# Kernel tuning notes

Hardware: AMD Instinct MI355X
Metric: run time of the kernel (lower is better)

Reference implementation:

```python
import jax, jax.numpy as jnp
import numpy as np

COS_EPS = 1e-6      # torch CosineSimilarity eps
NORM_EPS = 1e-12    # F.normalize default eps
NUM_HEADS = 4
TOPK = 5


def setup_inputs() -> dict:
    key = jax.random.key(0)
    ks = jax.random.split(key, 12)
    B, S, D_in, D = 32, 256, 768, 1024
    N = 50000
    sc = 0.02
    return {
        "hidden": jax.random.normal(ks[0], (B, S, D_in), jnp.float32),
        "table": jax.random.normal(ks[1], (N, D), jnp.float32),
        "fc1_w": jax.random.normal(ks[2], (D, D_in), jnp.float32) * sc,
        "fc1_b": jax.random.normal(ks[3], (D,), jnp.float32) * sc,
        "q_w": jax.random.normal(ks[4], (D, D), jnp.float32) * sc,
        "q_b": jax.random.normal(ks[5], (D,), jnp.float32) * sc,
        "k_w": jax.random.normal(ks[6], (D, D), jnp.float32) * sc,
        "k_b": jax.random.normal(ks[7], (D,), jnp.float32) * sc,
        "v_w": jax.random.normal(ks[8], (D, D), jnp.float32) * sc,
        "v_b": jax.random.normal(ks[9], (D,), jnp.float32) * sc,
        "out_w": jax.random.normal(ks[10], (D, D), jnp.float32) * sc,
        "out_b": jax.random.normal(ks[11], (D,), jnp.float32) * sc,
    }


def reference(hidden, table, fc1_w, fc1_b, q_w, q_b, k_w, k_b, v_w, v_b, out_w, out_b):
    B, S, _ = hidden.shape
    D = fc1_w.shape[0]
    H = NUM_HEADS
    hd = D // H

    # fc1 over last BERT hidden states: [B,S,1024]
    x = jnp.einsum("bsi,di->bsd", hidden, fc1_w) + fc1_b

    # ---- per-sample retrieval (vectorized over batch) ----
    m = jnp.mean(x, axis=1)                       # [B,D] mean over seq
    tn = jnp.linalg.norm(table, axis=1)           # [N]
    mn = jnp.linalg.norm(m, axis=1)               # [B]
    sim = (m @ table.T) / (jnp.maximum(mn, COS_EPS)[:, None]
                           * jnp.maximum(tn, COS_EPS)[None, :])  # [B,N]
    best = jnp.argmax(sim, axis=1)                # [B] top-1 cosine match

    tab_n = table / jnp.maximum(tn, NORM_EPS)[:, None]  # L2-normalized table
    sel = tab_n[best]                             # [B,D]
    # squared euclidean distance, expanded form (avoids [B,N,D] intermediate)
    d2 = (jnp.sum(sel * sel, axis=1)[:, None]
          - 2.0 * (sel @ tab_n.T)
          + jnp.sum(tab_n * tab_n, axis=1)[None, :])  # [B,N]
    _, idx = jax.lax.top_k(-d2, TOPK)             # 5 smallest distances
    targets = table[idx]                          # [B,5,D] (unnormalized rows)

    # ---- torch.nn.MultiheadAttention(query=targets, key=x, value=x) ----
    q = (jnp.einsum("bqd,ed->bqe", targets, q_w) + q_b).reshape(B, TOPK, H, hd)
    k = (jnp.einsum("bsd,ed->bse", x, k_w) + k_b).reshape(B, S, H, hd)
    v = (jnp.einsum("bsd,ed->bse", x, v_w) + v_b).reshape(B, S, H, hd)
    scores = jnp.einsum("bqhd,bkhd->bhqk", q, k) / jnp.sqrt(jnp.asarray(hd, x.dtype))
    attn = jax.nn.softmax(scores, axis=-1)        # [B,H,5,S]
    o = jnp.einsum("bhqk,bkhd->bqhd", attn, v).reshape(B, TOPK, D)
    attn_out = jnp.einsum("bqe,de->bqd", o, out_w) + out_b  # [B,5,D]

    return jnp.sum(attn_out, axis=1)              # [B,D]
```

## Files before the change

kernel.cpp:

```cpp
#include <hip/hip_runtime.h>
#include <stdint.h>

typedef short bf16x8 __attribute__((ext_vector_type(8)));
typedef float f32x4 __attribute__((ext_vector_type(4)));

#define NROWS 50000
#define BATCH 32
#define SEQ 256
#define DIN 768
#define DMODEL 1024
#define NTOPK 5
#define DOTS_RG 782
#define CHUNKF 64
#define NCHUNK_HALF 8

__device__ inline unsigned short f2bf(float f) {
  union { float f; unsigned u; } x; x.f = f;
  unsigned u = x.u;
  unsigned r = u + 0x7fffu + ((u >> 16) & 1u);
  return (unsigned short)(r >> 16);
}
__device__ inline float bf2f(unsigned short h) {
  union { unsigned u; float f; } x; x.u = ((unsigned)h) << 16; return x.f;
}
__device__ inline ushort4 cvt_hi4(float4 f) {
  ushort4 h; h.x = f2bf(f.x); h.y = f2bf(f.y); h.z = f2bf(f.z); h.w = f2bf(f.w); return h;
}
__device__ inline ushort4 cvt_lo4(float4 f, ushort4 h) {
  ushort4 l;
  l.x = f2bf(f.x - bf2f(h.x)); l.y = f2bf(f.y - bf2f(h.y));
  l.z = f2bf(f.z - bf2f(h.z)); l.w = f2bf(f.w - bf2f(h.w));
  return l;
}

__device__ __forceinline__ void gl_lds16(const void* g, void* l) {
  __builtin_amdgcn_global_load_lds(
      (const __attribute__((address_space(1))) unsigned int*)g,
      (__attribute__((address_space(3))) unsigned int*)l, 16, 0, 0);
}

__global__ void k_f32_to_bf16(const float* __restrict__ in, unsigned short* __restrict__ out, int n) {
  int i = (blockIdx.x * blockDim.x + threadIdx.x) * 4;
  int stride = gridDim.x * blockDim.x * 4;
  for (; i < n; i += stride) {
    float4 f = *(const float4*)(in + i);
    ushort4 o;
    o.x = f2bf(f.x); o.y = f2bf(f.y); o.z = f2bf(f.z); o.w = f2bf(f.w);
    *(ushort4*)(out + i) = o;
  }
}

__global__ void k_f32_to_bf16_3(const float* __restrict__ i0, unsigned short* __restrict__ o0, int n0,
                                const float* __restrict__ i1, unsigned short* __restrict__ o1, int n1,
                                const float* __restrict__ i2, unsigned short* __restrict__ o2, int n2) {
  int base = (blockIdx.x * blockDim.x + threadIdx.x) * 4;
  int stride = gridDim.x * blockDim.x * 4;
  for (int i = base; i < n0; i += stride) {
    float4 f = *(const float4*)(i0 + i);
    ushort4 o; o.x = f2bf(f.x); o.y = f2bf(f.y); o.z = f2bf(f.z); o.w = f2bf(f.w);
    *(ushort4*)(o0 + i) = o;
  }
  for (int i = base; i < n1; i += stride) {
    float4 f = *(const float4*)(i1 + i);
    ushort4 o; o.x = f2bf(f.x); o.y = f2bf(f.y); o.z = f2bf(f.z); o.w = f2bf(f.w);
    *(ushort4*)(o1 + i) = o;
  }
  for (int i = base; i < n2; i += stride) {
    float4 f = *(const float4*)(i2 + i);
    ushort4 o; o.x = f2bf(f.x); o.y = f2bf(f.y); o.z = f2bf(f.z); o.w = f2bf(f.w);
    *(ushort4*)(o2 + i) = o;
  }
}

__global__ void k_split_q(const float* __restrict__ v, unsigned short* __restrict__ qhi,
                          unsigned short* __restrict__ qlo) {
  int b = blockIdx.x;
  int e0 = threadIdx.x * 4;
  float4 f = *(const float4*)(v + (size_t)b * DMODEL + e0);
  ushort4 h = cvt_hi4(f);
  ushort4 l = cvt_lo4(f, h);
  *(ushort4*)(qhi + (size_t)b * DMODEL + e0) = h;
  *(ushort4*)(qlo + (size_t)b * DMODEL + e0) = l;
}

__global__ void k_mean_part(const float* __restrict__ hidden, float* __restrict__ hpart) {
  int b = blockIdx.x >> 3, tc = blockIdx.x & 7;
  int i = threadIdx.x;
  const float* p = hidden + ((size_t)b * SEQ + tc * 32) * DIN + i;
  float s = 0.f;
  #pragma unroll 4
  for (int t = 0; t < 32; ++t) s += p[t * DIN];
  hpart[((size_t)tc * 32 + b) * DIN + i] = s;
}
__global__ void k_mean_reduce(const float* __restrict__ hpart, float* __restrict__ hm) {
  int b = blockIdx.x;
  int i = threadIdx.x;
  float s = 0.f;
  #pragma unroll
  for (int tc = 0; tc < 8; ++tc) s += hpart[((size_t)tc * 32 + b) * DIN + i];
  hm[b * DIN + i] = s * (1.0f / SEQ);
}

__global__ void k_sgemm_wt(const float* __restrict__ A, const float* __restrict__ W,
                           const float* __restrict__ bias, float* __restrict__ C,
                           int M, int N, int K, float beta) {
  __shared__ float A_l[32][65];
  __shared__ float W_l[64][65];
  int tid = threadIdx.x;
  int tx = tid & 63, ty = tid >> 6;
  int n0 = blockIdx.x * 64, m0 = blockIdx.y * 32;
  float acc[8] = {0.f,0.f,0.f,0.f,0.f,0.f,0.f,0.f};
  for (int k0 = 0; k0 < K; k0 += 64) {
    #pragma unroll
    for (int i = 0; i < 8; ++i) {
      int idx = tid + 256 * i; int r = idx >> 6, c = idx & 63;
      A_l[r][c] = A[(size_t)(m0 + r) * K + k0 + c];
    }
    #pragma unroll
    for (int i = 0; i < 16; ++i) {
      int idx = tid + 256 * i; int r = idx >> 6, c = idx & 63;
      W_l[r][c] = W[(size_t)(n0 + r) * K + k0 + c];
    }
    __syncthreads();
    for (int kk = 0; kk < 64; ++kk) {
      float wv = W_l[tx][kk];
      #pragma unroll
      for (int r = 0; r < 8; ++r) acc[r] += A_l[ty * 8 + r][kk] * wv;
    }
    __syncthreads();
  }
  float bv = bias[n0 + tx] * beta;
  #pragma unroll
  for (int r = 0; r < 8; ++r) C[(size_t)(m0 + ty * 8 + r) * N + n0 + tx] = acc[r] + bv;
}

__global__ __launch_bounds__(256) void k_bf16_gemm(const unsigned short* __restrict__ A,
    const unsigned short* __restrict__ W, const float* __restrict__ bias,
    unsigned short* __restrict__ C, int M, int N, int K) {
  __shared__ unsigned short As[128][32];
  __shared__ unsigned short Ws[128][32];
  int tid = threadIdx.x;
  int wave = tid >> 6, lane = tid & 63;
  int wr = wave >> 1, wc = wave & 1;
  int bm = blockIdx.y * 128, bn = blockIdx.x * 128;
  int srow = lane >> 2;
  int scol = (lane & 3) * 8;
  f32x4 acc[4][4] = {};
  for (int k0 = 0; k0 < K; k0 += 32) {
    #pragma unroll
    for (int j = 0; j < 2; ++j) {
      int r0 = wave * 32 + j * 16;
      gl_lds16(A + (size_t)(bm + r0 + srow) * K + k0 + scol, &As[r0][0]);
      gl_lds16(W + (size_t)(bn + r0 + srow) * K + k0 + scol, &Ws[r0][0]);
    }
    __syncthreads();
    bf16x8 af[4], bfr[4];
    #pragma unroll
    for (int mi = 0; mi < 4; ++mi)
      af[mi] = *(const bf16x8*)(&As[wr * 64 + mi * 16 + (lane & 15)][(lane >> 4) * 8]);
    #pragma unroll
    for (int ni = 0; ni < 4; ++ni)
      bfr[ni] = *(const bf16x8*)(&Ws[wc * 64 + ni * 16 + (lane & 15)][(lane >> 4) * 8]);
    #pragma unroll
    for (int mi = 0; mi < 4; ++mi)
      #pragma unroll
      for (int ni = 0; ni < 4; ++ni)
        acc[mi][ni] = __builtin_amdgcn_mfma_f32_16x16x32_bf16(af[mi], bfr[ni], acc[mi][ni], 0, 0, 0);
    __syncthreads();
  }
  #pragma unroll
  for (int ni = 0; ni < 4; ++ni) {
    int col = bn + wc * 64 + ni * 16 + (lane & 15);
    float bv = bias[col];
    #pragma unroll
    for (int mi = 0; mi < 4; ++mi) {
      #pragma unroll
      for (int j = 0; j < 4; ++j) {
        int row = bm + wr * 64 + mi * 16 + (lane >> 4) * 4 + j;
        C[(size_t)row * N + col] = f2bf(acc[mi][ni][j] + bv);
      }
    }
  }
}

__global__ __launch_bounds__(256, 4) void k_dots(const float* __restrict__ table,
    const unsigned short* __restrict__ qhi, const unsigned short* __restrict__ qlo,
    float* __restrict__ normp, float* __restrict__ dotsg, int pass1) {
  __shared__ unsigned short As_hi[2][64 * 64];
  __shared__ unsigned short As_lo[2][64 * 64];
  __shared__ float npart[64][4];
  float* dot_lds = (float*)&As_hi[0][0];

  int tid = threadIdx.x;
  int wave = tid >> 6, lane = tid & 63;
  int rg = blockIdx.x >> 1, half = blockIdx.x & 1;
  int rbase = rg * 64;
  int kbase = half * 512;

  int r = tid >> 2;
  int q4 = tid & 3;
  int grow = rbase + r; if (grow >= NROWS) grow = NROWS - 1;
  const float* gsrc = table + (size_t)grow * DMODEL + kbase + q4 * 16;
  int wslot0 = ((q4 * 2) ^ (r & 7)) * 8;
  int wslot1 = ((q4 * 2 + 1) ^ (r & 7)) * 8;
  int wbase = r * 64;

  int abase = (wave * 16 + (lane & 15)) * 64;
  int al7 = lane & 7;
  const unsigned short* qh0 = qhi + (size_t)(lane & 15) * DMODEL + (lane >> 4) * 8 + kbase;
  const unsigned short* qh1 = qh0 + 16 * DMODEL;
  const unsigned short* ql0 = qlo + (size_t)(lane & 15) * DMODEL + (lane >> 4) * 8 + kbase;
  const unsigned short* ql1 = ql0 + 16 * DMODEL;

  float accn = 0.f;
  f32x4 acc0 = {}, acc1 = {};
  float4 f0, f1, f2, f3;

  auto LOAD = [&](int k0) {
    f0 = *(const float4*)(gsrc + k0);
    f1 = *(const float4*)(gsrc + k0 + 4);
    f2 = *(const float4*)(gsrc + k0 + 8);
    f3 = *(const float4*)(gsrc + k0 + 12);
  };
  auto WRITE = [&](int buf) {
    ushort4 h0 = cvt_hi4(f0), h1 = cvt_hi4(f1), h2 = cvt_hi4(f2), h3 = cvt_hi4(f3);
    ushort4 l0 = cvt_lo4(f0, h0), l1 = cvt_lo4(f1, h1), l2 = cvt_lo4(f2, h2), l3 = cvt_lo4(f3, h3);
    accn += f0.x*f0.x + f0.y*f0.y + f0.z*f0.z + f0.w*f0.w
          + f1.x*f1.x + f1.y*f1.y + f1.z*f1.z + f1.w*f1.w
          + f2.x*f2.x + f2.y*f2.y + f2.z*f2.z + f2.w*f2.w
          + f3.x*f3.x + f3.y*f3.y + f3.z*f3.z + f3.w*f3.w;
    *(ushort4*)&As_hi[buf][wbase + wslot0]     = h0;
    *(ushort4*)&As_hi[buf][wbase + wslot0 + 4] = h1;
    *(ushort4*)&As_hi[buf][wbase + wslot1]     = h2;
    *(ushort4*)&As_hi[buf][wbase + wslot1 + 4] = h3;
    *(ushort4*)&As_lo[buf][wbase + wslot0]     = l0;
    *(ushort4*)&As_lo[buf][wbase + wslot0 + 4] = l1;
    *(ushort4*)&As_lo[buf][wbase + wslot1]     = l2;
    *(ushort4*)&As_lo[buf][wbase + wslot1 + 4] = l3;
  };

  LOAD(0);
  for (int ch = 0; ch < NCHUNK_HALF; ++ch) {
    int buf = ch & 1;
    int k0 = ch * CHUNKF;
    bf16x8 bh0[2], bh1[2], bl0[2], bl1[2];
    #pragma unroll
    for (int kk = 0; kk < 2; ++kk) {
      int qoff = k0 + kk * 32;
      bh0[kk] = *(const bf16x8*)(qh0 + qoff);
      bh1[kk] = *(const bf16x8*)(qh1 + qoff);
      bl0[kk] = *(const bf16x8*)(ql0 + qoff);
      bl1[kk] = *(const bf16x8*)(ql1 + qoff);
    }
    WRITE(buf);
    if (ch + 1 < NCHUNK_HALF) LOAD(k0 + CHUNKF);
    #pragma unroll
    for (int kk = 0; kk < 2; ++kk) {
      int s = ((kk * 4 + (lane >> 4)) ^ al7) * 8;
      bf16x8 ah = *(const bf16x8*)&As_hi[buf][abase + s];
      bf16x8 al = *(const bf16x8*)&As_lo[buf][abase + s];
      acc0 = __builtin_amdgcn_mfma_f32_16x16x32_bf16(ah, bh0[kk], acc0, 0, 0, 0);
      acc1 = __builtin_amdgcn_mfma_f32_16x16x32_bf16(ah, bh1[kk], acc1, 0, 0, 0);
      acc0 = __builtin_amdgcn_mfma_f32_16x16x32_bf16(ah, bl0[kk], acc0, 0, 0, 0);
      acc1 = __builtin_amdgcn_mfma_f32_16x16x32_bf16(ah, bl1[kk], acc1, 0, 0, 0);
      acc0 = __builtin_amdgcn_mfma_f32_16x16x32_bf16(al, bh0[kk], acc0, 0, 0, 0);
      acc1 = __builtin_amdgcn_mfma_f32_16x16x32_bf16(al, bh1[kk], acc1, 0, 0, 0);
    }
  }

  npart[r][q4] = accn;
  __syncthreads();
  if (pass1 && tid < 64) {
    int rw = rbase + tid;
    if (rw < NROWS) {
      float n2 = npart[tid][0] + npart[tid][1] + npart[tid][2] + npart[tid][3];
      normp[(size_t)half * NROWS + rw] = n2;
    }
  }
  #pragma unroll
  for (int j = 0; j < 4; ++j) {
    int row = wave * 16 + (lane >> 4) * 4 + j;
    dot_lds[((lane & 15)) * 68 + row] = acc0[j];
    dot_lds[(16 + (lane & 15)) * 68 + row] = acc1[j];
  }
  __syncthreads();
  {
    int b = tid >> 3, r0 = (tid & 7) * 8;
    float* dst = dotsg + ((size_t)blockIdx.x * 32 + b) * 64 + r0;
    float4 v0 = *(const float4*)&dot_lds[b * 68 + r0];
    float4 v1 = *(const float4*)&dot_lds[b * 68 + r0 + 4];
    *(float4*)dst = v0;
    *(float4*)(dst + 4) = v1;
  }
}

__global__ void k_comb5(const float* __restrict__ dotsg, const float* __restrict__ normp,
                        float* __restrict__ norm2f, float* __restrict__ candv,
                        int* __restrict__ candi, int pass1, float eps) {
  __shared__ float sc[32 * 68];
  __shared__ float iv_lds[64];
  int rg = blockIdx.x;
  int tid = threadIdx.x;
  if (tid < 64) {
    int rw = rg * 64 + tid;
    int rc = rw < NROWS ? rw : NROWS - 1;
    float n2;
    if (pass1) {
      n2 = normp[rc] + normp[NROWS + rc];
      if (rw < NROWS) norm2f[rw] = n2;
    } else {
      n2 = norm2f[rc];
    }
    iv_lds[tid] = 1.0f / fmaxf(sqrtf(n2), eps);
  }
  __syncthreads();
  {
    int b = tid >> 3, r0 = (tid & 7) * 8;
    const float* p0 = dotsg + ((size_t)(rg * 2 + 0) * 32 + b) * 64 + r0;
    const float* p1 = dotsg + ((size_t)(rg * 2 + 1) * 32 + b) * 64 + r0;
    #pragma unroll
    for (int i = 0; i < 8; ++i)
      sc[b * 68 + r0 + i] = (p0[i] + p1[i]) * iv_lds[r0 + i];
  }
  __syncthreads();
  if (tid < 32) {
    float tv[5]; int ti[5];
    #pragma unroll
    for (int j = 0; j < 5; ++j) { tv[j] = -3.4e38f; ti[j] = 0x7fffffff; }
    int rbase = rg * 64;
    for (int rr = 0; rr < 64; ++rr) {
      int rw = rbase + rr;
      if (rw >= NROWS) break;
      float v = sc[tid * 68 + rr];
      if (v > tv[4] || (v == tv[4] && rw < ti[4])) {
        tv[4] = v; ti[4] = rw;
        #pragma unroll
        for (int j = 4; j > 0; --j) {
          bool sw = (tv[j] > tv[j-1]) || (tv[j] == tv[j-1] && ti[j] < ti[j-1]);
          if (sw) {
            float fv = tv[j]; tv[j] = tv[j-1]; tv[j-1] = fv;
            int ivx = ti[j]; ti[j] = ti[j-1]; ti[j-1] = ivx;
          }
        }
      }
    }
    #pragma unroll
    for (int j = 0; j < 5; ++j) {
      candv[((size_t)rg * 32 + tid) * 5 + j] = tv[j];
      candi[((size_t)rg * 32 + tid) * 5 + j] = ti[j];
    }
  }
}

__global__ void k_merge(const float* __restrict__ candv, const int* __restrict__ candi,
                        int* __restrict__ out_idx, int K, int nblk) {
  int b = blockIdx.x;
  int tid = threadIdx.x;
  float tv[5]; int ti[5];
  #pragma unroll
  for (int j = 0; j < 5; ++j) { tv[j] = -3.4e38f; ti[j] = 0x7fffffff; }
  for (int blk = tid; blk < nblk; blk += 256) {
    #pragma unroll
    for (int j = 0; j < 5; ++j) {
      float v = candv[((size_t)blk * 32 + b) * 5 + j];
      int idx = candi[((size_t)blk * 32 + b) * 5 + j];
      if (v > tv[4] || (v == tv[4] && idx < ti[4])) {
        tv[4] = v; ti[4] = idx;
        #pragma unroll
        for (int jj = 4; jj > 0; --jj) {
          bool sw = (tv[jj] > tv[jj-1]) || (tv[jj] == tv[jj-1] && ti[jj] < ti[jj-1]);
          if (sw) {
            float fv = tv[jj]; tv[jj] = tv[jj-1]; tv[jj-1] = fv;
            int ivx = ti[jj]; ti[jj] = ti[jj-1]; ti[jj-1] = ivx;
          }
        }
      }
    }
  }
  __shared__ float lv[256 * 5];
  __shared__ int   li[256 * 5];
  #pragma unroll
  for (int j = 0; j < 5; ++j) { lv[tid * 5 + j] = tv[j]; li[tid * 5 + j] = ti[j]; }
  __syncthreads();
  for (int off = 128; off >= 1; off >>= 1) {
    if (tid < off) {
      float av[5], bv[5]; int ai[5], bi[5];
      #pragma unroll
      for (int j = 0; j < 5; ++j) {
        av[j] = lv[tid * 5 + j]; ai[j] = li[tid * 5 + j];
        bv[j] = lv[(tid + off) * 5 + j]; bi[j] = li[(tid + off) * 5 + j];
      }
      int pa = 0, pb = 0;
      float mv[5]; int mi[5];
      #pragma unroll
      for (int j = 0; j < 5; ++j) {
        bool ta = (av[pa] > bv[pb]) || (av[pa] == bv[pb] && ai[pa] < bi[pb]);
        if (ta) { mv[j] = av[pa]; mi[j] = ai[pa]; ++pa; }
        else    { mv[j] = bv[pb]; mi[j] = bi[pb]; ++pb; }
      }
      #pragma unroll
      for (int j = 0; j < 5; ++j) { lv[tid * 5 + j] = mv[j]; li[tid * 5 + j] = mi[j]; }
    }
    __syncthreads();
  }
  if (tid == 0) {
    for (int j = 0; j < K; ++j) out_idx[b * K + j] = li[j];
  }
}

__global__ void k_gather_sel(const float* __restrict__ table, const int* __restrict__ best,
                             float* __restrict__ sel) {
  int b = blockIdx.x, e = threadIdx.x;
  int idx = best[b];
  sel[b * DMODEL + e] = table[(size_t)idx * DMODEL + e];
}

__global__ void k_gather_targets(const float* __restrict__ table, const int* __restrict__ idx5,
                                 float* __restrict__ tg) {
  int bt = blockIdx.x, e = threadIdx.x;
  int idx = idx5[bt];
  tg[(size_t)bt * DMODEL + e] = table[(size_t)idx * DMODEL + e];
}

__global__ __launch_bounds__(256) void k_attention(const float* __restrict__ q,
    const unsigned short* __restrict__ kb, const unsigned short* __restrict__ vb,
    float* __restrict__ obuf) {
  int bt = blockIdx.x;
  int b = bt / NTOPK;
  int tid = threadIdx.x;
  __shared__ float q_l[DMODEL];
  __shared__ float sc[4][SEQ];
  #pragma unroll
  for (int j = 0; j < 4; ++j) q_l[tid + 256 * j] = q[(size_t)bt * DMODEL + tid + 256 * j];
  __syncthreads();
  {
    int s = tid;
    const unsigned short* krow = kb + ((size_t)(b * SEQ + s)) * DMODEL;
    #pragma unroll
    for (int h = 0; h < 4; ++h) {
      float d = 0.f;
      for (int dd = 0; dd < 256; dd += 8) {
        uint4 pk = *(const uint4*)(krow + h * 256 + dd);
        const unsigned short* ph = (const unsigned short*)&pk;
        #pragma unroll
        for (int j2 = 0; j2 < 8; ++j2) d += bf2f(ph[j2]) * q_l[h * 256 + dd + j2];
      }
      sc[h][s] = d * 0.0625f;
    }
  }
  __syncthreads();
  {
    int h = tid >> 6, lane = tid & 63;
    float vals[4];
    float mx = -3.4e38f;
    #pragma unroll
    for (int j = 0; j < 4; ++j) { vals[j] = sc[h][lane + 64 * j]; mx = fmaxf(mx, vals[j]); }
    #pragma unroll
    for (int o = 1; o < 64; o <<= 1) mx = fmaxf(mx, __shfl_xor(mx, o));
    float sum = 0.f;
    #pragma unroll
    for (int j = 0; j < 4; ++j) { vals[j] = expf(vals[j] - mx); sum += vals[j]; }
    #pragma unroll
    for (int o = 1; o < 64; o <<= 1) sum += __shfl_xor(sum, o);
    float rz = 1.0f / sum;
    #pragma unroll
    for (int j = 0; j < 4; ++j) sc[h][lane + 64 * j] = vals[j] * rz;
  }
  __syncthreads();
  {
    int h = tid >> 6;
    int e0 = tid * 4;
    float a0 = 0.f, a1 = 0.f, a2 = 0.f, a3 = 0.f;
    const unsigned short* vbase = vb + (size_t)(b * SEQ) * DMODEL + e0;
    for (int s = 0; s < SEQ; ++s) {
      float w = sc[h][s];
      ushort4 v4 = *(const ushort4*)(vbase + (size_t)s * DMODEL);
      a0 += w * bf2f(v4.x); a1 += w * bf2f(v4.y); a2 += w * bf2f(v4.z); a3 += w * bf2f(v4.w);
    }
    float* op = obuf + (size_t)bt * DMODEL + e0;
    op[0] = a0; op[1] = a1; op[2] = a2; op[3] = a3;
  }
}

__global__ void k_osum(const float* __restrict__ obuf, float* __restrict__ osum) {
  int g = blockIdx.x * blockDim.x + threadIdx.x;
  if (g >= BATCH * DMODEL) return;
  int b = g >> 10, e = g & 1023;
  float s = 0.f;
  #pragma unroll
  for (int t = 0; t < NTOPK; ++t) s += obuf[(size_t)(b * NTOPK + t) * DMODEL + e];
  osum[g] = s;
}

extern "C" void kernel_launch(void* const* d_in, const int* in_sizes, int n_in,
                              void* d_out, int out_size, void* d_ws, size_t ws_size,
                              hipStream_t stream) {
  const float* hidden = (const float*)d_in[0];
  const float* table  = (const float*)d_in[1];
  const float* fc1_w  = (const float*)d_in[2];
  const float* fc1_b  = (const float*)d_in[3];
  const float* q_w    = (const float*)d_in[4];
  const float* q_b    = (const float*)d_in[5];
  const float* k_w    = (const float*)d_in[6];
  const float* k_b    = (const float*)d_in[7];
  const float* v_w    = (const float*)d_in[8];
  const float* v_b    = (const float*)d_in[9];
  const float* out_w  = (const float*)d_in[10];
  const float* out_b  = (const float*)d_in[11];
  float* out = (float*)d_out;

  char* ws = (char*)d_ws;
  size_t off = 0;
  auto alloc = [&](size_t bytes) -> void* {
    void* p = ws + off;
    off += (bytes + 255) & ~(size_t)255;
    return p;
  };
  unsigned short* hid_bf  = (unsigned short*)alloc((size_t)BATCH * SEQ * DIN * 2);
  unsigned short* fc1w_bf = (unsigned short*)alloc((size_t)DMODEL * DIN * 2);
  unsigned short* kw_bf   = (unsigned short*)alloc((size_t)DMODEL * DMODEL * 2);
  unsigned short* vw_bf   = (unsigned short*)alloc((size_t)DMODEL * DMODEL * 2);
  unsigned short* x_bf    = (unsigned short*)alloc((size_t)BATCH * SEQ * DMODEL * 2);
  unsigned short* k_bf    = (unsigned short*)alloc((size_t)BATCH * SEQ * DMODEL * 2);
  unsigned short* v_bf    = (unsigned short*)alloc((size_t)BATCH * SEQ * DMODEL * 2);
  unsigned short* qhi     = (unsigned short*)alloc((size_t)BATCH * DMODEL * 2);
  unsigned short* qlo     = (unsigned short*)alloc((size_t)BATCH * DMODEL * 2);
  float* hpart   = (float*)alloc((size_t)8 * BATCH * DIN * 4);
  float* hm      = (float*)alloc((size_t)BATCH * DIN * 4);
  float* m       = (float*)alloc((size_t)BATCH * DMODEL * 4);
  float* sel     = (float*)alloc((size_t)BATCH * DMODEL * 4);
  float* normp   = (float*)alloc((size_t)2 * NROWS * 4);
  float* norm2f  = (float*)alloc((size_t)NROWS * 4);
  float* dotsg   = (float*)alloc((size_t)DOTS_RG * 2 * 32 * 64 * 4);
  float* candv   = (float*)alloc((size_t)DOTS_RG * 32 * 5 * 4);
  int*   candi   = (int*)alloc((size_t)DOTS_RG * 32 * 5 * 4);
  int*   best    = (int*)alloc(BATCH * 4);
  int*   idx5    = (int*)alloc(BATCH * NTOPK * 4);
  float* targets = (float*)alloc((size_t)BATCH * NTOPK * DMODEL * 4);
  float* qbuf    = (float*)alloc((size_t)BATCH * NTOPK * DMODEL * 4);
  float* obuf    = (float*)alloc((size_t)BATCH * NTOPK * DMODEL * 4);
  float* osum    = (float*)alloc((size_t)BATCH * DMODEL * 4);
  (void)ws_size; (void)in_sizes; (void)n_in; (void)out_size;

  k_f32_to_bf16<<<2048, 256, 0, stream>>>(hidden, hid_bf, BATCH * SEQ * DIN);
  k_f32_to_bf16_3<<<1024, 256, 0, stream>>>(fc1_w, fc1w_bf, DMODEL * DIN,
                                            k_w, kw_bf, DMODEL * DMODEL,
                                            v_w, vw_bf, DMODEL * DMODEL);

  k_mean_part<<<256, 768, 0, stream>>>(hidden, hpart);
  k_mean_reduce<<<32, 768, 0, stream>>>(hpart, hm);
  k_sgemm_wt<<<dim3(16, 1), 256, 0, stream>>>(hm, fc1_w, fc1_b, m, 32, DMODEL, DIN, 1.0f);

  k_bf16_gemm<<<dim3(8, 64), 256, 0, stream>>>(hid_bf, fc1w_bf, fc1_b, x_bf, BATCH * SEQ, DMODEL, DIN);

  k_split_q<<<32, 256, 0, stream>>>(m, qhi, qlo);
  k_dots<<<DOTS_RG * 2, 256, 0, stream>>>(table, qhi, qlo, normp, dotsg, 1);
  k_comb5<<<DOTS_RG, 256, 0, stream>>>(dotsg, normp, norm2f, candv, candi, 1, 1e-6f);
  k_merge<<<32, 256, 0, stream>>>(candv, candi, best, 1, DOTS_RG);
  k_gather_sel<<<32, 1024, 0, stream>>>(table, best, sel);

  k_split_q<<<32, 256, 0, stream>>>(sel, qhi, qlo);
  k_dots<<<DOTS_RG * 2, 256, 0, stream>>>(table, qhi, qlo, normp, dotsg, 0);
  k_comb5<<<DOTS_RG, 256, 0, stream>>>(dotsg, normp, norm2f, candv, candi, 0, 1e-12f);
  k_merge<<<32, 256, 0, stream>>>(candv, candi, idx5, NTOPK, DOTS_RG);
  k_gather_targets<<<160, 1024, 0, stream>>>(table, idx5, targets);

  k_sgemm_wt<<<dim3(16, 5), 256, 0, stream>>>(targets, q_w, q_b, qbuf, BATCH * NTOPK, DMODEL, DMODEL, 1.0f);

  k_bf16_gemm<<<dim3(8, 64), 256, 0, stream>>>(x_bf, kw_bf, k_b, k_bf, BATCH * SEQ, DMODEL, DMODEL);
  k_bf16_gemm<<<dim3(8, 64), 256, 0, stream>>>(x_bf, vw_bf, v_b, v_bf, BATCH * SEQ, DMODEL, DMODEL);

  k_attention<<<160, 256, 0, stream>>>(qbuf, k_bf, v_bf, obuf);
  k_osum<<<128, 256, 0, stream>>>(obuf, osum);
  k_sgemm_wt<<<dim3(16, 1), 256, 0, stream>>>(osum, out_w, out_b, out, 32, DMODEL, DMODEL, 5.0f);
}
```

Measured before the change: 584.2 us.

## Fuse small prep, merge, gather and split kernels; cut k_dots LDS for occupancy

The hidden-state bf16 conversion now shares one pass with the per-chunk seq sum, so hidden is read once instead of twice. The q hi/lo split moves into the fc1 sgemm epilogue and into a combined merge+gather kernel, and the top-5 merge writes targets directly. The osum reduction moves into the out-proj sgemm A-load. k_dots drops LDS double-buffering to a single buffer, raises launch bounds to 6 blocks, and loads the q fragments inside the inner loop. Fewer launches and more resident blocks are traded against less overlap of LDS writes with MFMA reads in k_dots.

```diff
diff --git a/kernel.cpp b/kernel.cpp
--- a/kernel.cpp
+++ b/kernel.cpp
@@ -39,15 +39,29 @@
       (__attribute__((address_space(3))) unsigned int*)l, 16, 0, 0);
 }
 
-__global__ void k_f32_to_bf16(const float* __restrict__ in, unsigned short* __restrict__ out, int n) {
-  int i = (blockIdx.x * blockDim.x + threadIdx.x) * 4;
-  int stride = gridDim.x * blockDim.x * 4;
-  for (; i < n; i += stride) {
-    float4 f = *(const float4*)(in + i);
-    ushort4 o;
-    o.x = f2bf(f.x); o.y = f2bf(f.y); o.z = f2bf(f.z); o.w = f2bf(f.w);
-    *(ushort4*)(out + i) = o;
-  }
+__global__ void k_hidden_prep(const float* __restrict__ hidden, unsigned short* __restrict__ hid_bf,
+                              float* __restrict__ hpart) {
+  int b = blockIdx.x >> 3, tc = blockIdx.x & 7;
+  int i = threadIdx.x;
+  const float* p = hidden + ((size_t)b * SEQ + tc * 32) * DIN + i;
+  unsigned short* o = hid_bf + ((size_t)b * SEQ + tc * 32) * DIN + i;
+  float s = 0.f;
+  #pragma unroll 4
+  for (int t = 0; t < 32; ++t) {
+    float v = p[t * DIN];
+    s += v;
+    o[t * DIN] = f2bf(v);
+  }
+  hpart[((size_t)tc * 32 + b) * DIN + i] = s;
+}
+
+__global__ void k_mean_reduce(const float* __restrict__ hpart, float* __restrict__ hm) {
+  int b = blockIdx.x;
+  int i = threadIdx.x;
+  float s = 0.f;
+  #pragma unroll
+  for (int tc = 0; tc < 8; ++tc) s += hpart[((size_t)tc * 32 + b) * DIN + i];
+  hm[b * DIN + i] = s * (1.0f / SEQ);
 }
 
 __global__ void k_f32_to_bf16_3(const float* __restrict__ i0, unsigned short* __restrict__ o0, int n0,
@@ -72,38 +86,10 @@
   }
 }
 
-__global__ void k_split_q(const float* __restrict__ v, unsigned short* __restrict__ qhi,
-                          unsigned short* __restrict__ qlo) {
-  int b = blockIdx.x;
-  int e0 = threadIdx.x * 4;
-  float4 f = *(const float4*)(v + (size_t)b * DMODEL + e0);
-  ushort4 h = cvt_hi4(f);
-  ushort4 l = cvt_lo4(f, h);
-  *(ushort4*)(qhi + (size_t)b * DMODEL + e0) = h;
-  *(ushort4*)(qlo + (size_t)b * DMODEL + e0) = l;
-}
-
-__global__ void k_mean_part(const float* __restrict__ hidden, float* __restrict__ hpart) {
-  int b = blockIdx.x >> 3, tc = blockIdx.x & 7;
-  int i = threadIdx.x;
-  const float* p = hidden + ((size_t)b * SEQ + tc * 32) * DIN + i;
-  float s = 0.f;
-  #pragma unroll 4
-  for (int t = 0; t < 32; ++t) s += p[t * DIN];
-  hpart[((size_t)tc * 32 + b) * DIN + i] = s;
-}
-__global__ void k_mean_reduce(const float* __restrict__ hpart, float* __restrict__ hm) {
-  int b = blockIdx.x;
-  int i = threadIdx.x;
-  float s = 0.f;
-  #pragma unroll
-  for (int tc = 0; tc < 8; ++tc) s += hpart[((size_t)tc * 32 + b) * DIN + i];
-  hm[b * DIN + i] = s * (1.0f / SEQ);
-}
-
 __global__ void k_sgemm_wt(const float* __restrict__ A, const float* __restrict__ W,
                            const float* __restrict__ bias, float* __restrict__ C,
-                           int M, int N, int K, float beta) {
+                           int M, int N, int K, float beta, int sum5,
+                           unsigned short* __restrict__ qhi, unsigned short* __restrict__ qlo) {
   __shared__ float A_l[32][65];
   __shared__ float W_l[64][65];
   int tid = threadIdx.x;
@@ -114,7 +100,15 @@
     #pragma unroll
     for (int i = 0; i < 8; ++i) {
       int idx = tid + 256 * i; int r = idx >> 6, c = idx & 63;
-      A_l[r][c] = A[(size_t)(m0 + r) * K + k0 + c];
+      if (sum5) {
+        float s = 0.f;
+        #pragma unroll
+        for (int t = 0; t < 5; ++t)
+          s += A[((size_t)(m0 + r) * 5 + t) * K + k0 + c];
+        A_l[r][c] = s;
+      } else {
+        A_l[r][c] = A[(size_t)(m0 + r) * K + k0 + c];
+      }
     }
     #pragma unroll
     for (int i = 0; i < 16; ++i) {
@@ -131,7 +125,16 @@
   }
   float bv = bias[n0 + tx] * beta;
   #pragma unroll
-  for (int r = 0; r < 8; ++r) C[(size_t)(m0 + ty * 8 + r) * N + n0 + tx] = acc[r] + bv;
+  for (int r = 0; r < 8; ++r) {
+    int row = m0 + ty * 8 + r, col = n0 + tx;
+    float v = acc[r] + bv;
+    C[(size_t)row * N + col] = v;
+    if (qhi) {
+      unsigned short h = f2bf(v);
+      qhi[(size_t)row * N + col] = h;
+      qlo[(size_t)row * N + col] = f2bf(v - bf2f(h));
+    }
+  }
 }
 
 __global__ __launch_bounds__(256) void k_bf16_gemm(const unsigned short* __restrict__ A,
@@ -183,13 +186,12 @@
   }
 }
 
-__global__ __launch_bounds__(256, 4) void k_dots(const float* __restrict__ table,
+__global__ __launch_bounds__(256, 6) void k_dots(const float* __restrict__ table,
     const unsigned short* __restrict__ qhi, const unsigned short* __restrict__ qlo,
     float* __restrict__ normp, float* __restrict__ dotsg, int pass1) {
-  __shared__ unsigned short As_hi[2][64 * 64];
-  __shared__ unsigned short As_lo[2][64 * 64];
+  __shared__ unsigned short As[2][64 * 64];
   __shared__ float npart[64][4];
-  float* dot_lds = (float*)&As_hi[0][0];
+  float* dot_lds = (float*)&As[0][0];
 
   int tid = threadIdx.x;
   int wave = tid >> 6, lane = tid & 63;
@@ -222,49 +224,44 @@
     f2 = *(const float4*)(gsrc + k0 + 8);
     f3 = *(const float4*)(gsrc + k0 + 12);
   };
-  auto WRITE = [&](int buf) {
+  auto WRITE = [&]() {
     ushort4 h0 = cvt_hi4(f0), h1 = cvt_hi4(f1), h2 = cvt_hi4(f2), h3 = cvt_hi4(f3);
     ushort4 l0 = cvt_lo4(f0, h0), l1 = cvt_lo4(f1, h1), l2 = cvt_lo4(f2, h2), l3 = cvt_lo4(f3, h3);
     accn += f0.x*f0.x + f0.y*f0.y + f0.z*f0.z + f0.w*f0.w
           + f1.x*f1.x + f1.y*f1.y + f1.z*f1.z + f1.w*f1.w
           + f2.x*f2.x + f2.y*f2.y + f2.z*f2.z + f2.w*f2.w
           + f3.x*f3.x + f3.y*f3.y + f3.z*f3.z + f3.w*f3.w;
-    *(ushort4*)&As_hi[buf][wbase + wslot0]     = h0;
-    *(ushort4*)&As_hi[buf][wbase + wslot0 + 4] = h1;
-    *(ushort4*)&As_hi[buf][wbase + wslot1]     = h2;
-    *(ushort4*)&As_hi[buf][wbase + wslot1 + 4] = h3;
-    *(ushort4*)&As_lo[buf][wbase + wslot0]     = l0;
-    *(ushort4*)&As_lo[buf][wbase + wslot0 + 4] = l1;
-    *(ushort4*)&As_lo[buf][wbase + wslot1]     = l2;
-    *(ushort4*)&As_lo[buf][wbase + wslot1 + 4] = l3;
+    *(ushort4*)&As[0][wbase + wslot0]     = h0;
+    *(ushort4*)&As[0][wbase + wslot0 + 4] = h1;
+    *(ushort4*)&As[0][wbase + wslot1]     = h2;
+    *(ushort4*)&As[0][wbase + wslot1 + 4] = h3;
+    *(ushort4*)&As[1][wbase + wslot0]     = l0;
+    *(ushort4*)&As[1][wbase + wslot0 + 4] = l1;
+    *(ushort4*)&As[1][wbase + wslot1]     = l2;
+    *(ushort4*)&As[1][wbase + wslot1 + 4] = l3;
   };
 
   LOAD(0);
   for (int ch = 0; ch < NCHUNK_HALF; ++ch) {
-    int buf = ch & 1;
     int k0 = ch * CHUNKF;
-    bf16x8 bh0[2], bh1[2], bl0[2], bl1[2];
-    #pragma unroll
-    for (int kk = 0; kk < 2; ++kk) {
-      int qoff = k0 + kk * 32;
-      bh0[kk] = *(const bf16x8*)(qh0 + qoff);
-      bh1[kk] = *(const bf16x8*)(qh1 + qoff);
-      bl0[kk] = *(const bf16x8*)(ql0 + qoff);
-      bl1[kk] = *(const bf16x8*)(ql1 + qoff);
-    }
-    WRITE(buf);
+    WRITE();
     if (ch + 1 < NCHUNK_HALF) LOAD(k0 + CHUNKF);
     #pragma unroll
     for (int kk = 0; kk < 2; ++kk) {
       int s = ((kk * 4 + (lane >> 4)) ^ al7) * 8;
-      bf16x8 ah = *(const bf16x8*)&As_hi[buf][abase + s];
-      bf16x8 al = *(const bf16x8*)&As_lo[buf][abase + s];
-      acc0 = __builtin_amdgcn_mfma_f32_16x16x32_bf16(ah, bh0[kk], acc0, 0, 0, 0);
-      acc1 = __builtin_amdgcn_mfma_f32_16x16x32_bf16(ah, bh1[kk], acc1, 0, 0, 0);
-      acc0 = __builtin_amdgcn_mfma_f32_16x16x32_bf16(ah, bl0[kk], acc0, 0, 0, 0);
-      acc1 = __builtin_amdgcn_mfma_f32_16x16x32_bf16(ah, bl1[kk], acc1, 0, 0, 0);
-      acc0 = __builtin_amdgcn_mfma_f32_16x16x32_bf16(al, bh0[kk], acc0, 0, 0, 0);
-      acc1 = __builtin_amdgcn_mfma_f32_16x16x32_bf16(al, bh1[kk], acc1, 0, 0, 0);
+      bf16x8 ah = *(const bf16x8*)&As[0][abase + s];
+      bf16x8 al = *(const bf16x8*)&As[1][abase + s];
+      int qoff = k0 + kk * 32;
+      bf16x8 bh0 = *(const bf16x8*)(qh0 + qoff);
+      bf16x8 bh1 = *(const bf16x8*)(qh1 + qoff);
+      bf16x8 bl0 = *(const bf16x8*)(ql0 + qoff);
+      bf16x8 bl1 = *(const bf16x8*)(ql1 + qoff);
+      acc0 = __builtin_amdgcn_mfma_f32_16x16x32_bf16(ah, bh0, acc0, 0, 0, 0);
+      acc1 = __builtin_amdgcn_mfma_f32_16x16x32_bf16(ah, bh1, acc1, 0, 0, 0);
+      acc0 = __builtin_amdgcn_mfma_f32_16x16x32_bf16(ah, bl0, acc0, 0, 0, 0);
+      acc1 = __builtin_amdgcn_mfma_f32_16x16x32_bf16(ah, bl1, acc1, 0, 0, 0);
+      acc0 = __builtin_amdgcn_mfma_f32_16x16x32_bf16(al, bh0, acc0, 0, 0, 0);
+      acc1 = __builtin_amdgcn_mfma_f32_16x16x32_bf16(al, bh1, acc1, 0, 0, 0);
     }
   }
 
@@ -352,14 +349,46 @@
   }
 }
 
-__global__ void k_merge(const float* __restrict__ candv, const int* __restrict__ candi,
-                        int* __restrict__ out_idx, int K, int nblk) {
+__global__ void k_mg_split(const float* __restrict__ candv, const int* __restrict__ candi,
+                           const float* __restrict__ table, unsigned short* __restrict__ qhi,
+                           unsigned short* __restrict__ qlo) {
   int b = blockIdx.x;
   int tid = threadIdx.x;
+  float bv = -3.4e38f; int bi = 0x7fffffff;
+  for (int blk = tid; blk < DOTS_RG; blk += 256) {
+    float v = candv[((size_t)blk * 32 + b) * 5];
+    int idx = candi[((size_t)blk * 32 + b) * 5];
+    if (v > bv || (v == bv && idx < bi)) { bv = v; bi = idx; }
+  }
+  __shared__ float sv[256];
+  __shared__ int   si[256];
+  sv[tid] = bv; si[tid] = bi;
+  __syncthreads();
+  for (int off = 128; off >= 1; off >>= 1) {
+    if (tid < off) {
+      float v2 = sv[tid + off]; int i2 = si[tid + off];
+      if (v2 > sv[tid] || (v2 == sv[tid] && i2 < si[tid])) { sv[tid] = v2; si[tid] = i2; }
+    }
+    __syncthreads();
+  }
+  int best = si[0];
+  const float* row = table + (size_t)best * DMODEL;
+  int e0 = tid * 4;
+  float4 f = *(const float4*)(row + e0);
+  ushort4 h = cvt_hi4(f);
+  ushort4 l = cvt_lo4(f, h);
+  *(ushort4*)(qhi + (size_t)b * DMODEL + e0) = h;
+  *(ushort4*)(qlo + (size_t)b * DMODEL + e0) = l;
+}
+
+__global__ void k_mg5(const float* __restrict__ candv, const int* __restrict__ candi,
+                      const float* __restrict__ table, float* __restrict__ targets) {
+  int b = blockIdx.x;
+  int tid = threadIdx.x;
   float tv[5]; int ti[5];
   #pragma unroll
   for (int j = 0; j < 5; ++j) { tv[j] = -3.4e38f; ti[j] = 0x7fffffff; }
-  for (int blk = tid; blk < nblk; blk += 256) {
+  for (int blk = tid; blk < DOTS_RG; blk += 256) {
     #pragma unroll
     for (int j = 0; j < 5; ++j) {
       float v = candv[((size_t)blk * 32 + b) * 5 + j];
@@ -403,23 +432,13 @@
     }
     __syncthreads();
   }
-  if (tid == 0) {
-    for (int j = 0; j < K; ++j) out_idx[b * K + j] = li[j];
-  }
-}
-
-__global__ void k_gather_sel(const float* __restrict__ table, const int* __restrict__ best,
-                             float* __restrict__ sel) {
-  int b = blockIdx.x, e = threadIdx.x;
-  int idx = best[b];
-  sel[b * DMODEL + e] = table[(size_t)idx * DMODEL + e];
-}
-
-__global__ void k_gather_targets(const float* __restrict__ table, const int* __restrict__ idx5,
-                                 float* __restrict__ tg) {
-  int bt = blockIdx.x, e = threadIdx.x;
-  int idx = idx5[bt];
-  tg[(size_t)bt * DMODEL + e] = table[(size_t)idx * DMODEL + e];
+  #pragma unroll
+  for (int j = 0; j < 5; ++j) {
+    int idx = li[j];
+    const float* row = table + (size_t)idx * DMODEL;
+    for (int e = tid * 4; e < DMODEL; e += 1024)
+      *(float4*)(targets + ((size_t)b * NTOPK + j) * DMODEL + e) = *(const float4*)(row + e);
+  }
 }
 
 __global__ __launch_bounds__(256) void k_attention(const float* __restrict__ q,
@@ -480,16 +499,6 @@
     float* op = obuf + (size_t)bt * DMODEL + e0;
     op[0] = a0; op[1] = a1; op[2] = a2; op[3] = a3;
   }
-}
-
-__global__ void k_osum(const float* __restrict__ obuf, float* __restrict__ osum) {
-  int g = blockIdx.x * blockDim.x + threadIdx.x;
-  if (g >= BATCH * DMODEL) return;
-  int b = g >> 10, e = g & 1023;
-  float s = 0.f;
-  #pragma unroll
-  for (int t = 0; t < NTOPK; ++t) s += obuf[(size_t)(b * NTOPK + t) * DMODEL + e];
-  osum[g] = s;
 }
 
 extern "C" void kernel_launch(void* const* d_in, const int* in_sizes, int n_in,
@@ -528,49 +537,42 @@
   float* hpart   = (float*)alloc((size_t)8 * BATCH * DIN * 4);
   float* hm      = (float*)alloc((size_t)BATCH * DIN * 4);
   float* m       = (float*)alloc((size_t)BATCH * DMODEL * 4);
-  float* sel     = (float*)alloc((size_t)BATCH * DMODEL * 4);
   float* normp   = (float*)alloc((size_t)2 * NROWS * 4);
   float* norm2f  = (float*)alloc((size_t)NROWS * 4);
   float* dotsg   = (float*)alloc((size_t)DOTS_RG * 2 * 32 * 64 * 4);
   float* candv   = (float*)alloc((size_t)DOTS_RG * 32 * 5 * 4);
   int*   candi   = (int*)alloc((size_t)DOTS_RG * 32 * 5 * 4);
-  int*   best    = (int*)alloc(BATCH * 4);
-  int*   idx5    = (int*)alloc(BATCH * NTOPK * 4);
   float* targets = (float*)alloc((size_t)BATCH * NTOPK * DMODEL * 4);
   float* qbuf    = (float*)alloc((size_t)BATCH * NTOPK * DMODEL * 4);
   float* obuf    = (float*)alloc((size_t)BATCH * NTOPK * DMODEL * 4);
-  float* osum    = (float*)alloc((size_t)BATCH * DMODEL * 4);
   (void)ws_size; (void)in_sizes; (void)n_in; (void)out_size;
 
-  k_f32_to_bf16<<<2048, 256, 0, stream>>>(hidden, hid_bf, BATCH * SEQ * DIN);
+  k_hidden_prep<<<256, 768, 0, stream>>>(hidden, hid_bf, hpart);
   k_f32_to_bf16_3<<<1024, 256, 0, stream>>>(fc1_w, fc1w_bf, DMODEL * DIN,
                                             k_w, kw_bf, DMODEL * DMODEL,
                                             v_w, vw_bf, DMODEL * DMODEL);
-
-  k_mean_part<<<256, 768, 0, stream>>>(hidden, hpart);
   k_mean_reduce<<<32, 768, 0, stream>>>(hpart, hm);
-  k_sgemm_wt<<<dim3(16, 1), 256, 0, stream>>>(hm, fc1_w, fc1_b, m, 32, DMODEL, DIN, 1.0f);
+
+  k_sgemm_wt<<<dim3(16, 1), 256, 0, stream>>>(hm, fc1_w, fc1_b, m, 32, DMODEL, DIN, 1.0f,
+                                              0, qhi, qlo);
 
   k_bf16_gemm<<<dim3(8, 64), 256, 0, stream>>>(hid_bf, fc1w_bf, fc1_b, x_bf, BATCH * SEQ, DMODEL, DIN);
 
-  k_split_q<<<32, 256, 0, stream>>>(m, qhi, qlo);
   k_dots<<<DOTS_RG * 2, 256, 0, stream>>>(table, qhi, qlo, normp, dotsg, 1);
   k_comb5<<<DOTS_RG, 256, 0, stream>>>(dotsg, normp, norm2f, candv, candi, 1, 1e-6f);
-  k_merge<<<32, 256, 0, stream>>>(candv, candi, best, 1, DOTS_RG);
-  k_gather_sel<<<32, 1024, 0, stream>>>(table, best, sel);
-
-  k_split_q<<<32, 256, 0, stream>>>(sel, qhi, qlo);
+  k_mg_split<<<32, 256, 0, stream>>>(candv, candi, table, qhi, qlo);
+
   k_dots<<<DOTS_RG * 2, 256, 0, stream>>>(table, qhi, qlo, normp, dotsg, 0);
   k_comb5<<<DOTS_RG, 256, 0, stream>>>(dotsg, normp, norm2f, candv, candi, 0, 1e-12f);
-  k_merge<<<32, 256, 0, stream>>>(candv, candi, idx5, NTOPK, DOTS_RG);
-  k_gather_targets<<<160, 1024, 0, stream>>>(table, idx5, targets);
-
-  k_sgemm_wt<<<dim3(16, 5), 256, 0, stream>>>(targets, q_w, q_b, qbuf, BATCH * NTOPK, DMODEL, DMODEL, 1.0f);
+  k_mg5<<<32, 256, 0, stream>>>(candv, candi, table, targets);
+
+  k_sgemm_wt<<<dim3(16, 5), 256, 0, stream>>>(targets, q_w, q_b, qbuf, BATCH * NTOPK, DMODEL, DMODEL,
+                                              1.0f, 0, nullptr, nullptr);
 
   k_bf16_gemm<<<dim3(8, 64), 256, 0, stream>>>(x_bf, kw_bf, k_b, k_bf, BATCH * SEQ, DMODEL, DMODEL);
   k_bf16_gemm<<<dim3(8, 64), 256, 0, stream>>>(x_bf, vw_bf, v_b, v_bf, BATCH * SEQ, DMODEL, DMODEL);
 
   k_attention<<<160, 256, 0, stream>>>(qbuf, k_bf, v_bf, obuf);
-  k_osum<<<128, 256, 0, stream>>>(obuf, osum);
-  k_sgemm_wt<<<dim3(16, 1), 256, 0, stream>>>(osum, out_w, out_b, out, 32, DMODEL, DMODEL, 5.0f);
-}
+  k_sgemm_wt<<<dim3(16, 1), 256, 0, stream>>>(obuf, out_w, out_b, out, 32, DMODEL, DMODEL,
+                                              5.0f, 1, nullptr, nullptr);
+}
```

Result: slower. 676.2 us (+15.8%).

## Precompute bf16 hi/lo split table and norms once, reuse in both dot passes

Applied to the files above, without the earlier changes.

Adds a prep kernel that converts the fp32 table into bf16 hi/lo arrays and computes row squared norms once. Both retrieval dot passes then read the presplit bf16 directly from global memory, without the LDS staging or in-kernel conversion. This moves conversion work out of the dot kernels and simplifies comb5. The cost is an extra full read and write of the table, and the dot passes now read as many bytes as the fp32 table each time, so total memory traffic grows.

```diff
diff --git a/kernel.cpp b/kernel.cpp
--- a/kernel.cpp
+++ b/kernel.cpp
@@ -11,8 +11,6 @@
 #define DMODEL 1024
 #define NTOPK 5
 #define DOTS_RG 782
-#define CHUNKF 64
-#define NCHUNK_HALF 8
 
 __device__ inline unsigned short f2bf(float f) {
   union { float f; unsigned u; } x; x.f = f;
@@ -70,6 +68,29 @@
     ushort4 o; o.x = f2bf(f.x); o.y = f2bf(f.y); o.z = f2bf(f.z); o.w = f2bf(f.w);
     *(ushort4*)(o2 + i) = o;
   }
+}
+
+__global__ __launch_bounds__(256) void k_table_prep(const float* __restrict__ table,
+    unsigned short* __restrict__ tabhi, unsigned short* __restrict__ tablo,
+    float* __restrict__ norm2f) {
+  int row = blockIdx.x * 4 + (threadIdx.x >> 6);
+  int lane = threadIdx.x & 63;
+  if (row >= NROWS) return;
+  const float* src = table + (size_t)row * DMODEL;
+  float accn = 0.f;
+  #pragma unroll
+  for (int i = 0; i < 4; ++i) {
+    int e = (lane + i * 64) * 4;
+    float4 f = *(const float4*)(src + e);
+    ushort4 h = cvt_hi4(f);
+    ushort4 l = cvt_lo4(f, h);
+    accn += f.x * f.x + f.y * f.y + f.z * f.z + f.w * f.w;
+    *(ushort4*)(tabhi + (size_t)row * DMODEL + e) = h;
+    *(ushort4*)(tablo + (size_t)row * DMODEL + e) = l;
+  }
+  #pragma unroll
+  for (int o = 1; o < 64; o <<= 1) accn += __shfl_xor(accn, o);
+  if (lane == 0) norm2f[row] = accn;
 }
 
 __global__ void k_split_q(const float* __restrict__ v, unsigned short* __restrict__ qhi,
@@ -183,105 +204,48 @@
   }
 }
 
-__global__ __launch_bounds__(256, 4) void k_dots(const float* __restrict__ table,
-    const unsigned short* __restrict__ qhi, const unsigned short* __restrict__ qlo,
-    float* __restrict__ normp, float* __restrict__ dotsg, int pass1) {
-  __shared__ unsigned short As_hi[2][64 * 64];
-  __shared__ unsigned short As_lo[2][64 * 64];
-  __shared__ float npart[64][4];
-  float* dot_lds = (float*)&As_hi[0][0];
-
+__global__ __launch_bounds__(256, 4) void k_dots(const unsigned short* __restrict__ tabhi,
+    const unsigned short* __restrict__ tablo, const unsigned short* __restrict__ qhi,
+    const unsigned short* __restrict__ qlo, float* __restrict__ dotsg) {
+  __shared__ float dot_lds[32 * 68];
   int tid = threadIdx.x;
   int wave = tid >> 6, lane = tid & 63;
   int rg = blockIdx.x >> 1, half = blockIdx.x & 1;
   int rbase = rg * 64;
   int kbase = half * 512;
 
-  int r = tid >> 2;
-  int q4 = tid & 3;
-  int grow = rbase + r; if (grow >= NROWS) grow = NROWS - 1;
-  const float* gsrc = table + (size_t)grow * DMODEL + kbase + q4 * 16;
-  int wslot0 = ((q4 * 2) ^ (r & 7)) * 8;
-  int wslot1 = ((q4 * 2 + 1) ^ (r & 7)) * 8;
-  int wbase = r * 64;
-
-  int abase = (wave * 16 + (lane & 15)) * 64;
-  int al7 = lane & 7;
+  int row = rbase + wave * 16 + (lane & 15);
+  if (row >= NROWS) row = NROWS - 1;
+  const unsigned short* th = tabhi + (size_t)row * DMODEL + kbase + (lane >> 4) * 8;
+  const unsigned short* tl = tablo + (size_t)row * DMODEL + kbase + (lane >> 4) * 8;
   const unsigned short* qh0 = qhi + (size_t)(lane & 15) * DMODEL + (lane >> 4) * 8 + kbase;
   const unsigned short* qh1 = qh0 + 16 * DMODEL;
   const unsigned short* ql0 = qlo + (size_t)(lane & 15) * DMODEL + (lane >> 4) * 8 + kbase;
   const unsigned short* ql1 = ql0 + 16 * DMODEL;
 
-  float accn = 0.f;
   f32x4 acc0 = {}, acc1 = {};
-  float4 f0, f1, f2, f3;
-
-  auto LOAD = [&](int k0) {
-    f0 = *(const float4*)(gsrc + k0);
-    f1 = *(const float4*)(gsrc + k0 + 4);
-    f2 = *(const float4*)(gsrc + k0 + 8);
-    f3 = *(const float4*)(gsrc + k0 + 12);
-  };
-  auto WRITE = [&](int buf) {
-    ushort4 h0 = cvt_hi4(f0), h1 = cvt_hi4(f1), h2 = cvt_hi4(f2), h3 = cvt_hi4(f3);
-    ushort4 l0 = cvt_lo4(f0, h0), l1 = cvt_lo4(f1, h1), l2 = cvt_lo4(f2, h2), l3 = cvt_lo4(f3, h3);
-    accn += f0.x*f0.x + f0.y*f0.y + f0.z*f0.z + f0.w*f0.w
-          + f1.x*f1.x + f1.y*f1.y + f1.z*f1.z + f1.w*f1.w
-          + f2.x*f2.x + f2.y*f2.y + f2.z*f2.z + f2.w*f2.w
-          + f3.x*f3.x + f3.y*f3.y + f3.z*f3.z + f3.w*f3.w;
-    *(ushort4*)&As_hi[buf][wbase + wslot0]     = h0;
-    *(ushort4*)&As_hi[buf][wbase + wslot0 + 4] = h1;
-    *(ushort4*)&As_hi[buf][wbase + wslot1]     = h2;
-    *(ushort4*)&As_hi[buf][wbase + wslot1 + 4] = h3;
-    *(ushort4*)&As_lo[buf][wbase + wslot0]     = l0;
-    *(ushort4*)&As_lo[buf][wbase + wslot0 + 4] = l1;
-    *(ushort4*)&As_lo[buf][wbase + wslot1]     = l2;
-    *(ushort4*)&As_lo[buf][wbase + wslot1 + 4] = l3;
-  };
-
-  LOAD(0);
-  for (int ch = 0; ch < NCHUNK_HALF; ++ch) {
-    int buf = ch & 1;
-    int k0 = ch * CHUNKF;
-    bf16x8 bh0[2], bh1[2], bl0[2], bl1[2];
-    #pragma unroll
-    for (int kk = 0; kk < 2; ++kk) {
-      int qoff = k0 + kk * 32;
-      bh0[kk] = *(const bf16x8*)(qh0 + qoff);
-      bh1[kk] = *(const bf16x8*)(qh1 + qoff);
-      bl0[kk] = *(const bf16x8*)(ql0 + qoff);
-      bl1[kk] = *(const bf16x8*)(ql1 + qoff);
-    }
-    WRITE(buf);
-    if (ch + 1 < NCHUNK_HALF) LOAD(k0 + CHUNKF);
-    #pragma unroll
-    for (int kk = 0; kk < 2; ++kk) {
-      int s = ((kk * 4 + (lane >> 4)) ^ al7) * 8;
-      bf16x8 ah = *(const bf16x8*)&As_hi[buf][abase + s];
-      bf16x8 al = *(const bf16x8*)&As_lo[buf][abase + s];
-      acc0 = __builtin_amdgcn_mfma_f32_16x16x32_bf16(ah, bh0[kk], acc0, 0, 0, 0);
-      acc1 = __builtin_amdgcn_mfma_f32_16x16x32_bf16(ah, bh1[kk], acc1, 0, 0, 0);
-      acc0 = __builtin_amdgcn_mfma_f32_16x16x32_bf16(ah, bl0[kk], acc0, 0, 0, 0);
-      acc1 = __builtin_amdgcn_mfma_f32_16x16x32_bf16(ah, bl1[kk], acc1, 0, 0, 0);
-      acc0 = __builtin_amdgcn_mfma_f32_16x16x32_bf16(al, bh0[kk], acc0, 0, 0, 0);
-      acc1 = __builtin_amdgcn_mfma_f32_16x16x32_bf16(al, bh1[kk], acc1, 0, 0, 0);
-    }
-  }
-
-  npart[r][q4] = accn;
-  __syncthreads();
-  if (pass1 && tid < 64) {
-    int rw = rbase + tid;
-    if (rw < NROWS) {
-      float n2 = npart[tid][0] + npart[tid][1] + npart[tid][2] + npart[tid][3];
-      normp[(size_t)half * NROWS + rw] = n2;
-    }
-  }
+  #pragma unroll 4
+  for (int ks = 0; ks < 16; ++ks) {
+    int off = ks * 32;
+    bf16x8 ah  = *(const bf16x8*)(th + off);
+    bf16x8 al  = *(const bf16x8*)(tl + off);
+    bf16x8 bh0 = *(const bf16x8*)(qh0 + off);
+    bf16x8 bh1 = *(const bf16x8*)(qh1 + off);
+    bf16x8 bl0 = *(const bf16x8*)(ql0 + off);
+    bf16x8 bl1 = *(const bf16x8*)(ql1 + off);
+    acc0 = __builtin_amdgcn_mfma_f32_16x16x32_bf16(ah, bh0, acc0, 0, 0, 0);
+    acc1 = __builtin_amdgcn_mfma_f32_16x16x32_bf16(ah, bh1, acc1, 0, 0, 0);
+    acc0 = __builtin_amdgcn_mfma_f32_16x16x32_bf16(ah, bl0, acc0, 0, 0, 0);
+    acc1 = __builtin_amdgcn_mfma_f32_16x16x32_bf16(ah, bl1, acc1, 0, 0, 0);
+    acc0 = __builtin_amdgcn_mfma_f32_16x16x32_bf16(al, bh0, acc0, 0, 0, 0);
+    acc1 = __builtin_amdgcn_mfma_f32_16x16x32_bf16(al, bh1, acc1, 0, 0, 0);
+  }
+
   #pragma unroll
   for (int j = 0; j < 4; ++j) {
-    int row = wave * 16 + (lane >> 4) * 4 + j;
-    dot_lds[((lane & 15)) * 68 + row] = acc0[j];
-    dot_lds[(16 + (lane & 15)) * 68 + row] = acc1[j];
+    int r = wave * 16 + (lane >> 4) * 4 + j;
+    dot_lds[((lane & 15)) * 68 + r] = acc0[j];
+    dot_lds[(16 + (lane & 15)) * 68 + r] = acc1[j];
   }
   __syncthreads();
   {
@@ -294,9 +258,8 @@
   }
 }
 
-__global__ void k_comb5(const float* __restrict__ dotsg, const float* __restrict__ normp,
-                        float* __restrict__ norm2f, float* __restrict__ candv,
-                        int* __restrict__ candi, int pass1, float eps) {
+__global__ void k_comb5(const float* __restrict__ dotsg, const float* __restrict__ norm2f,
+                        float* __restrict__ candv, int* __restrict__ candi, float eps) {
   __shared__ float sc[32 * 68];
   __shared__ float iv_lds[64];
   int rg = blockIdx.x;
@@ -304,14 +267,7 @@
   if (tid < 64) {
     int rw = rg * 64 + tid;
     int rc = rw < NROWS ? rw : NROWS - 1;
-    float n2;
-    if (pass1) {
-      n2 = normp[rc] + normp[NROWS + rc];
-      if (rw < NROWS) norm2f[rw] = n2;
-    } else {
-      n2 = norm2f[rc];
-    }
-    iv_lds[tid] = 1.0f / fmaxf(sqrtf(n2), eps);
+    iv_lds[tid] = 1.0f / fmaxf(sqrtf(norm2f[rc]), eps);
   }
   __syncthreads();
   {
@@ -525,11 +481,12 @@
   unsigned short* v_bf    = (unsigned short*)alloc((size_t)BATCH * SEQ * DMODEL * 2);
   unsigned short* qhi     = (unsigned short*)alloc((size_t)BATCH * DMODEL * 2);
   unsigned short* qlo     = (unsigned short*)alloc((size_t)BATCH * DMODEL * 2);
+  unsigned short* tabhi   = (unsigned short*)alloc((size_t)NROWS * DMODEL * 2);
+  unsigned short* tablo   = (unsigned short*)alloc((size_t)NROWS * DMODEL * 2);
   float* hpart   = (float*)alloc((size_t)8 * BATCH * DIN * 4);
   float* hm      = (float*)alloc((size_t)BATCH * DIN * 4);
   float* m       = (float*)alloc((size_t)BATCH * DMODEL * 4);
   float* sel     = (float*)alloc((size_t)BATCH * DMODEL * 4);
-  float* normp   = (float*)alloc((size_t)2 * NROWS * 4);
   float* norm2f  = (float*)alloc((size_t)NROWS * 4);
   float* dotsg   = (float*)alloc((size_t)DOTS_RG * 2 * 32 * 64 * 4);
   float* candv   = (float*)alloc((size_t)DOTS_RG * 32 * 5 * 4);
@@ -546,6 +503,7 @@
   k_f32_to_bf16_3<<<1024, 256, 0, stream>>>(fc1_w, fc1w_bf, DMODEL * DIN,
                                             k_w, kw_bf, DMODEL * DMODEL,
                                             v_w, vw_bf, DMODEL * DMODEL);
+  k_table_prep<<<12500, 256, 0, stream>>>(table, tabhi, tablo, norm2f);
 
   k_mean_part<<<256, 768, 0, stream>>>(hidden, hpart);
   k_mean_reduce<<<32, 768, 0, stream>>>(hpart, hm);
@@ -554,14 +512,14 @@
   k_bf16_gemm<<<dim3(8, 64), 256, 0, stream>>>(hid_bf, fc1w_bf, fc1_b, x_bf, BATCH * SEQ, DMODEL, DIN);
 
   k_split_q<<<32, 256, 0, stream>>>(m, qhi, qlo);
-  k_dots<<<DOTS_RG * 2, 256, 0, stream>>>(table, qhi, qlo, normp, dotsg, 1);
-  k_comb5<<<DOTS_RG, 256, 0, stream>>>(dotsg, normp, norm2f, candv, candi, 1, 1e-6f);
+  k_dots<<<DOTS_RG * 2, 256, 0, stream>>>(tabhi, tablo, qhi, qlo, dotsg);
+  k_comb5<<<DOTS_RG, 256, 0, stream>>>(dotsg, norm2f, candv, candi, 1e-6f);
   k_merge<<<32, 256, 0, stream>>>(candv, candi, best, 1, DOTS_RG);
   k_gather_sel<<<32, 1024, 0, stream>>>(table, best, sel);
 
   k_split_q<<<32, 256, 0, stream>>>(sel, qhi, qlo);
-  k_dots<<<DOTS_RG * 2, 256, 0, stream>>>(table, qhi, qlo, normp, dotsg, 0);
-  k_comb5<<<DOTS_RG, 256, 0, stream>>>(dotsg, normp, norm2f, candv, candi, 0, 1e-12f);
+  k_dots<<<DOTS_RG * 2, 256, 0, stream>>>(tabhi, tablo, qhi, qlo, dotsg);
+  k_comb5<<<DOTS_RG, 256, 0, stream>>>(dotsg, norm2f, candv, candi, 1e-12f);
   k_merge<<<32, 256, 0, stream>>>(candv, candi, idx5, NTOPK, DOTS_RG);
   k_gather_targets<<<160, 1024, 0, stream>>>(table, idx5, targets);
 
```

Result: slower. 692.2 us (+18.5%).
